# Performance work log

Hardware: AMD Instinct MI355X
Metric: run time of the kernel (lower is better)

Reference implementation:

```python
import jax, jax.numpy as jnp
import numpy as np

B, S = 64, 32
VF, IF = 512, 256
F = VF + IF        # fused feature dim == sensory dim
U = 768            # wiring units == rnn_hidden_dim (motor_size == units)
UNFOLDS = 6        # ncps LTC default ode_unfolds
EPS = 1e-8


def setup_inputs() -> dict:
    key = jax.random.key(0)
    ks = jax.random.split(key, 24)
    d = {}
    d['fv'] = jax.random.normal(ks[0], (B, S, VF), jnp.float32)
    d['fv_alter'] = jax.random.normal(ks[1], (B, S, VF), jnp.float32)
    d['fi'] = jax.random.normal(ks[2], (B, S, IF), jnp.float32)
    d['dec'] = jax.random.normal(ks[3], (B, S, 2), jnp.float32)
    # strictly increasing timestamps so relative timespans are positive
    d['ts'] = jnp.cumsum(jax.random.uniform(ks[4], (B, S + 1), jnp.float32, 0.01, 0.1), axis=1)
    # LTC cell parameters (ncps init ranges), FullyConnected wiring -> dense masks of ones
    d['input_w'] = jnp.ones((F,), jnp.float32)
    d['input_b'] = jnp.zeros((F,), jnp.float32)
    d['sensory_mu'] = jax.random.uniform(ks[5], (F, U), jnp.float32, 0.3, 0.8)
    d['sensory_sigma'] = jax.random.uniform(ks[6], (F, U), jnp.float32, 3.0, 8.0)
    d['sensory_w'] = jax.random.uniform(ks[7], (F, U), jnp.float32, 0.001, 1.0)
    d['sensory_erev'] = jnp.sign(jax.random.normal(ks[8], (F, U), jnp.float32))
    d['mu'] = jax.random.uniform(ks[9], (U, U), jnp.float32, 0.3, 0.8)
    d['sigma'] = jax.random.uniform(ks[10], (U, U), jnp.float32, 3.0, 8.0)
    d['w'] = jax.random.uniform(ks[11], (U, U), jnp.float32, 0.001, 1.0)
    d['erev'] = jnp.sign(jax.random.normal(ks[12], (U, U), jnp.float32))
    d['gleak'] = jax.random.uniform(ks[13], (U,), jnp.float32, 0.001, 1.0)
    d['vleak'] = jax.random.uniform(ks[14], (U,), jnp.float32, -0.2, 0.2)
    d['cm'] = jax.random.uniform(ks[15], (U,), jnp.float32, 0.4, 0.6)
    d['output_w'] = jnp.ones((U,), jnp.float32)
    d['output_b'] = jnp.zeros((U,), jnp.float32)
    d['W1'] = jax.random.normal(ks[16], (U, 128), jnp.float32) / np.sqrt(U)
    d['b1'] = jnp.zeros((128,), jnp.float32)
    d['W2'] = jax.random.normal(ks[17], (128, 6), jnp.float32) / np.sqrt(128.0)
    d['b2'] = jnp.zeros((6,), jnp.float32)
    return d


def _ltc(fused, rel_ts, input_w, input_b, sensory_mu, sensory_sigma, sensory_w,
         sensory_erev, mu, sigma, w, erev, gleak, vleak, cm, output_w, output_b):
    b = fused.shape[0]
    h0 = jnp.zeros((b, U), fused.dtype)

    def step(v, xs):
        inp, elapsed = xs  # (B,F), (B,)
        x = inp * input_w + input_b
        # sensory synapse activations: (B, F, U)
        s_act = sensory_w * jax.nn.sigmoid(sensory_sigma * (x[:, :, None] - sensory_mu))
        w_num_s = jnp.einsum('bfu,fu->bu', s_act, sensory_erev)
        w_den_s = jnp.sum(s_act, axis=1)
        cm_t = cm / (elapsed[:, None] / UNFOLDS)  # (B,U)

        def unfold(vv, _):
            act = w * jax.nn.sigmoid(sigma * (vv[:, :, None] - mu))  # (B,U,U)
            num = jnp.einsum('buv,uv->bv', act, erev) + w_num_s
            den = jnp.sum(act, axis=1) + w_den_s
            vv = (cm_t * vv + gleak * vleak + num) / (cm_t + gleak + den + EPS)
            return vv, None

        v, _ = jax.lax.scan(unfold, v, None, length=UNFOLDS)
        out = v * output_w + output_b  # motor_size == units
        return v, out

    _, outs = jax.lax.scan(step, h0, (jnp.swapaxes(fused, 0, 1), rel_ts.T))
    return jnp.swapaxes(outs, 0, 1), h0  # (B,S,U)


def reference(fv, fv_alter, fi, dec, ts, input_w, input_b, sensory_mu, sensory_sigma,
              sensory_w, sensory_erev, mu, sigma, w, erev, gleak, vleak, cm,
              output_w, output_b, W1, b1, W2, b2):
    fused = jnp.concatenate([fv, fi], axis=-1)  # FusionModule 'cat'
    rel_ts = ts[:, 1:] - ts[:, :-1]
    h_seq, h0 = _ltc(fused, rel_ts, input_w, input_b, sensory_mu, sensory_sigma,
                     sensory_w, sensory_erev, mu, sigma, w, erev, gleak, vleak, cm,
                     output_w, output_b)
    x = (h_seq - h0[:, None, :]) @ W1 + b1
    x = jnp.where(x > 0, x, 0.1 * x)  # LeakyReLU(0.1)
    pose = x @ W2 + b2
    return pose[:, None], h_seq  # (B,1,S,6), (B,S,U)
```

## Files before the change

### kernel.cpp

```cpp
#include <hip/hip_runtime.h>

#define Bq 64
#define Sq 32
#define VFq 512
#define IFq 256
#define Fq 768
#define Uq 768
#define UNFq 6
#define L2E 1.44269504088896340736f

template <int CTRL>
__device__ __forceinline__ float dpp_add(float x) {
  int t = __builtin_amdgcn_update_dpp(0, __builtin_bit_cast(int, x), CTRL, 0xF, 0xF, true);
  return x + __builtin_bit_cast(float, t);
}
__device__ __forceinline__ float swz_add4(float x) {
  int t = __builtin_amdgcn_ds_swizzle(__builtin_bit_cast(int, x), 0x101F);
  return x + __builtin_bit_cast(float, t);
}

__global__ __launch_bounds__(256) void k_prep(
    const float* __restrict__ smu, const float* __restrict__ ssig,
    const float* __restrict__ sw,  const float* __restrict__ ser,
    const float* __restrict__ rmu, const float* __restrict__ rsig,
    const float* __restrict__ rw,  const float* __restrict__ rer,
    const float* __restrict__ ts,
    float4* __restrict__ Ps, float4* __restrict__ Pr,
    float* __restrict__ iel, unsigned* __restrict__ flags)
{
  int bid = blockIdx.x, tid = threadIdx.x;
  if (bid < 1152) {
    int set = bid / 576, tile = bid % 576;
    int tv = tile / 24, tu = tile % 24;
    const float* Amu = set ? rmu : smu;
    const float* Asg = set ? rsig : ssig;
    const float* Aw  = set ? rw  : sw;
    const float* Aer = set ? rer : ser;
    float4* P = set ? Pr : Ps;
    __shared__ float4 tl[32][33];
    int cu = tid & 31, r0 = tid >> 5;
    for (int rr = 0; rr < 32; rr += 8) {
      int v = tv*32 + r0 + rr, u = tu*32 + cu;
      int idx = v*Uq + u;
      float sg = Asg[idx], m = Amu[idx], ww = Aw[idx], er = Aer[idx];
      tl[cu][r0+rr] = make_float4(-sg*L2E, sg*m*L2E, ww, ww*er);
    }
    __syncthreads();
    for (int rr = 0; rr < 32; rr += 8) {
      int u = tu*32 + r0 + rr, v = tv*32 + (tid & 31);
      P[u*Fq + v] = tl[r0+rr][tid & 31];
    }
  } else {
    for (int i = tid; i < Bq*Sq; i += 256) {
      int b = i / Sq, t = i % Sq;
      iel[i] = (float)UNFq / (ts[b*(Sq+1)+t+1] - ts[b*(Sq+1)+t]);
    }
    for (int i = tid; i < 512; i += 256) flags[i] = 0u;
  }
}

__global__ __launch_bounds__(768) void k_sensory(
    const float* __restrict__ fv, const float* __restrict__ fi,
    const float* __restrict__ iw, const float* __restrict__ ib,
    const float4* __restrict__ Ps,
    float* __restrict__ wns, float* __restrict__ wds)
{
  __shared__ float xs[16][Fq];
  __shared__ float scr[12][8][33];
  int tid = threadIdx.x;
  int bt_tile = blockIdx.x >> 6;
  int ut = blockIdx.x & 63;
  int u0 = ut * 12, bt0 = bt_tile * 16;
  {
    float wv = iw[tid], bv = ib[tid];
    for (int j = 0; j < 16; ++j) {
      int bt = bt0 + j, b = bt >> 5, t = bt & 31;
      float raw = (tid < VFq) ? fv[(b*Sq + t)*VFq + tid]
                              : fi[(b*Sq + t)*IFq + (tid - VFq)];
      xs[j][tid] = raw * wv + bv;
    }
  }
  __syncthreads();
  int w = tid >> 6, l = tid & 63;
  const float4* P = Ps + (u0 + w)*Fq;
  #pragma unroll
  for (int pass = 0; pass < 4; ++pass) {
    float num[4], den[4];
    #pragma unroll
    for (int q = 0; q < 4; ++q) { num[q] = 0.f; den[q] = 0.f; }
    for (int i = 0; i < 12; ++i) {
      int f = l + 64*i;
      float4 p = P[f];
      #pragma unroll
      for (int q = 0; q < 4; ++q) {
        float arg = fmaf(p.x, xs[4*pass + q][f], p.y);
        float e = __builtin_amdgcn_exp2f(arg);
        float r = __builtin_amdgcn_rcpf(1.0f + e);
        den[q] = fmaf(p.z, r, den[q]);
        num[q] = fmaf(p.w, r, num[q]);
      }
    }
    #pragma unroll
    for (int q = 0; q < 4; ++q) {
      num[q] = dpp_add<0xB1>(num[q]); den[q] = dpp_add<0xB1>(den[q]);
      num[q] = dpp_add<0x4E>(num[q]); den[q] = dpp_add<0x4E>(den[q]);
      num[q] = swz_add4(num[q]);      den[q] = swz_add4(den[q]);
    }
    if ((l & 7) == 0) {
      int rep = l >> 3;
      #pragma unroll
      for (int q = 0; q < 4; ++q) {
        scr[w][rep][4*pass + q] = num[q];
        scr[w][rep][16 + 4*pass + q] = den[q];
      }
    }
    __builtin_amdgcn_sched_barrier(0);
  }
  __syncthreads();
  if (tid < 192) {
    int u = tid >> 4, j = tid & 15;
    float nt = 0.f, dt = 0.f;
    #pragma unroll
    for (int rep = 0; rep < 8; ++rep) { nt += scr[u][rep][j]; dt += scr[u][rep][16+j]; }
    int bt = bt0 + j, b = bt >> 5, t = bt & 31;
    wns[(t*Bq + b)*Uq + (u0 + u)] = nt;
    wds[(t*Bq + b)*Uq + (u0 + u)] = dt;
  }
}

__global__ __launch_bounds__(768)
void k_recurrent(
    const float4* __restrict__ Pr,
    const float* __restrict__ wns, const float* __restrict__ wds,
    float* __restrict__ vg, const float* __restrict__ iel,
    unsigned* __restrict__ flags,
    const float* __restrict__ gleak, const float* __restrict__ vleak,
    const float* __restrict__ cm, const float* __restrict__ ow,
    const float* __restrict__ ob, float* __restrict__ hout)
{
  __shared__ float4 vvP[4][Uq];
  __shared__ float2 scr2[12][8][9];
  __shared__ float sinv[16][Sq];
  __shared__ float swn[2][96], swd[2][96];
  __shared__ float sgl[12], sglvl[12], scm[12], sow[12], sob[12];
  int tid = threadIdx.x;
  int g = blockIdx.x >> 6;
  int ut = blockIdx.x & 63;
  int u0 = ut*12, b0 = g*16;
  if (tid < 512) { int j = tid >> 5, t = tid & 31; sinv[j][t] = iel[(b0+j)*Sq + t]; }
  if (tid < 12) {
    float gl0 = gleak[u0+tid];
    sgl[tid] = gl0; sglvl[tid] = gl0 * vleak[u0+tid];
    scm[tid] = cm[u0+tid]; sow[tid] = ow[u0+tid]; sob[tid] = ob[u0+tid];
  }
  #pragma unroll
  for (int p = 0; p < 4; ++p) vvP[p][tid] = make_float4(0.f, 0.f, 0.f, 0.f);
  int w = tid >> 6, l = tid & 63;
  float4 Prg[12];
  #pragma unroll
  for (int i = 0; i < 12; ++i) Prg[i] = Pr[(u0 + w)*Uq + l + 64*i];
  __syncthreads();
  int uu = tid >> 3, jv = tid & 7;
  int p = 1;
  for (int t = 0; t < Sq; ++t) {
    if (tid < 96) {
      swn[0][tid] = wns[(t*Bq + b0 + jv)*Uq + u0 + uu];
      swd[0][tid] = wds[(t*Bq + b0 + jv)*Uq + u0 + uu];
      swn[1][tid] = wns[(t*Bq + b0 + 8 + jv)*Uq + u0 + uu];
      swd[1][tid] = wds[(t*Bq + b0 + 8 + jv)*Uq + u0 + uu];
    }
    for (int k = 0; k < UNFq; ++k, ++p) {
      int sp = p & 1, rp = sp ^ 1;
      #pragma unroll
      for (int h = 0; h < 2; ++h) {
        if (p > 1) {
          const unsigned* f = flags + (h*4 + g)*64 + l;
          unsigned tgt = (unsigned)(p - 1);
          while (true) {
            unsigned vf = __hip_atomic_load(f, __ATOMIC_RELAXED, __HIP_MEMORY_SCOPE_AGENT);
            if (__ballot(vf < tgt) == 0ull) break;
            __builtin_amdgcn_s_sleep(1);
          }
          const unsigned long long* src = (const unsigned long long*)
              (vg + (((rp*2 + h)*4 + g)*Uq + tid)*8);
          float2 tmp[4];
          #pragma unroll
          for (int q = 0; q < 4; ++q) {
            unsigned long long uq = __hip_atomic_load(src + q, __ATOMIC_RELAXED,
                                                      __HIP_MEMORY_SCOPE_AGENT);
            tmp[q] = __builtin_bit_cast(float2, uq);
          }
          vvP[2*h+0][tid] = make_float4(tmp[0].x, tmp[0].y, tmp[1].x, tmp[1].y);
          vvP[2*h+1][tid] = make_float4(tmp[2].x, tmp[2].y, tmp[3].x, tmp[3].y);
        }
        __syncthreads();
        #pragma unroll
        for (int pass = 0; pass < 2; ++pass) {
          int pn = 2*h + pass;
          float num[4], den[4];
          #pragma unroll
          for (int q = 0; q < 4; ++q) { num[q] = 0.f; den[q] = 0.f; }
          #pragma unroll
          for (int i = 0; i < 12; ++i) {
            int v = l + 64*i;
            float4 pp = Prg[i];
            float4 y = vvP[pn][v];
            float a0 = fmaf(pp.x, y.x, pp.y);
            float a1 = fmaf(pp.x, y.y, pp.y);
            float a2 = fmaf(pp.x, y.z, pp.y);
            float a3 = fmaf(pp.x, y.w, pp.y);
            float r0 = __builtin_amdgcn_rcpf(1.0f + __builtin_amdgcn_exp2f(a0));
            float r1 = __builtin_amdgcn_rcpf(1.0f + __builtin_amdgcn_exp2f(a1));
            float r2 = __builtin_amdgcn_rcpf(1.0f + __builtin_amdgcn_exp2f(a2));
            float r3 = __builtin_amdgcn_rcpf(1.0f + __builtin_amdgcn_exp2f(a3));
            den[0] = fmaf(pp.z, r0, den[0]);
            num[0] = fmaf(pp.w, r0, num[0]);
            den[1] = fmaf(pp.z, r1, den[1]);
            num[1] = fmaf(pp.w, r1, num[1]);
            den[2] = fmaf(pp.z, r2, den[2]);
            num[2] = fmaf(pp.w, r2, num[2]);
            den[3] = fmaf(pp.z, r3, den[3]);
            num[3] = fmaf(pp.w, r3, num[3]);
          }
          #pragma unroll
          for (int q = 0; q < 4; ++q) {
            num[q] = dpp_add<0xB1>(num[q]); den[q] = dpp_add<0xB1>(den[q]);
            num[q] = dpp_add<0x4E>(num[q]); den[q] = dpp_add<0x4E>(den[q]);
            num[q] = swz_add4(num[q]);      den[q] = swz_add4(den[q]);
          }
          if ((l & 7) == 0) {
            int r = l >> 3;
            #pragma unroll
            for (int q = 0; q < 4; ++q)
              scr2[w][r][4*pass + q] = make_float2(num[q], den[q]);
          }
          __builtin_amdgcn_sched_barrier(0);
        }
        __syncthreads();
        if (tid < 96) {
          float nt = swn[h][tid], dt = swd[h][tid];
          #pragma unroll
          for (int r = 0; r < 8; ++r) { float2 s = scr2[uu][r][jv]; nt += s.x; dt += s.y; }
          int jh = h*8 + jv;
          float cmt = scm[uu] * sinv[jh][t];
          const float* vrow = (const float*)&vvP[2*h + (jv >> 2)][u0 + uu];
          float vold = vrow[jv & 3];
          float vnew = (cmt*vold + sglvl[uu] + nt)
                     * __builtin_amdgcn_rcpf(cmt + sgl[uu] + dt + 1e-8f);
          __hip_atomic_store(&vg[(((sp*2 + h)*4 + g)*Uq + u0 + uu)*8 + jv], vnew,
                             __ATOMIC_RELAXED, __HIP_MEMORY_SCOPE_AGENT);
          if (k == UNFq-1)
            hout[((b0 + jh)*Sq + t)*Uq + u0 + uu] = fmaf(vnew, sow[uu], sob[uu]);
        }
        __builtin_amdgcn_s_waitcnt(0);
        __syncthreads();
        if (tid == 0)
          __hip_atomic_store(&flags[(h*4 + g)*64 + ut], (unsigned)p,
                             __ATOMIC_RELAXED, __HIP_MEMORY_SCOPE_AGENT);
      }
    }
  }
}

__global__ __launch_bounds__(128) void k_head(
    const float* __restrict__ hseq, const float* __restrict__ W1,
    const float* __restrict__ b1, const float* __restrict__ W2,
    const float* __restrict__ b2, float* __restrict__ pose)
{
  __shared__ float h[Uq];
  __shared__ float x1[128];
  int bt = blockIdx.x, tid = threadIdx.x;
  for (int j = 0; j < 6; ++j) h[tid + 128*j] = hseq[bt*Uq + tid + 128*j];
  __syncthreads();
  float acc = b1[tid];
  for (int f = 0; f < Uq; ++f) acc = fmaf(h[f], W1[f*128 + tid], acc);
  x1[tid] = acc > 0.f ? acc : 0.1f*acc;
  __syncthreads();
  if (tid < 6) {
    float a2 = b2[tid];
    #pragma unroll
    for (int c = 0; c < 128; ++c) a2 = fmaf(x1[c], W2[c*6 + tid], a2);
    pose[bt*6 + tid] = a2;
  }
}

extern "C" void kernel_launch(void* const* d_in, const int* in_sizes, int n_in,
                              void* d_out, int out_size, void* d_ws, size_t ws_size,
                              hipStream_t stream) {
  const float* fv   = (const float*)d_in[0];
  const float* fi   = (const float*)d_in[2];
  const float* ts   = (const float*)d_in[4];
  const float* iw   = (const float*)d_in[5];
  const float* ibb  = (const float*)d_in[6];
  const float* smu  = (const float*)d_in[7];
  const float* ssig = (const float*)d_in[8];
  const float* sw   = (const float*)d_in[9];
  const float* ser  = (const float*)d_in[10];
  const float* rmu  = (const float*)d_in[11];
  const float* rsig = (const float*)d_in[12];
  const float* rw   = (const float*)d_in[13];
  const float* rer  = (const float*)d_in[14];
  const float* gl   = (const float*)d_in[15];
  const float* vl   = (const float*)d_in[16];
  const float* cm   = (const float*)d_in[17];
  const float* ow   = (const float*)d_in[18];
  const float* ob   = (const float*)d_in[19];
  const float* W1   = (const float*)d_in[20];
  const float* b1   = (const float*)d_in[21];
  const float* W2   = (const float*)d_in[22];
  const float* b2   = (const float*)d_in[23];

  float* pose = (float*)d_out;
  float* hseq = (float*)d_out + Bq*Sq*6;

  float* ws = (float*)d_ws;
  float4* Ps = (float4*)ws;
  float4* Pr = (float4*)(ws + 2359296);
  float* wns = ws + 4718592;
  float* wds = ws + 6291456;
  float* vg  = ws + 7864320;
  float* iel = ws + 7962624;
  unsigned* flags = (unsigned*)(ws + 7964672);

  k_prep<<<1153, 256, 0, stream>>>(smu, ssig, sw, ser, rmu, rsig, rw, rer,
                                   ts, Ps, Pr, iel, flags);
  k_sensory<<<8192, 768, 0, stream>>>(fv, fi, iw, ibb, Ps, wns, wds);
  k_recurrent<<<256, 768, 0, stream>>>(Pr, wns, wds, vg, iel, flags,
                                       gl, vl, cm, ow, ob, hseq);
  k_head<<<2048, 128, 0, stream>>>(hseq, W1, b1, W2, b2, pose);
}
```

Baseline: 2.794 ms.

## Split recurrent kernel into more batch groups and share reciprocal across sigmoid pairs

The recurrent kernel now gives each block 8 batch rows instead of 16 and launches 512 blocks instead of 256. Each block does one pass per half instead of two, which shortens the serial per-unfold critical path, at the cost of more blocks polling flags and more grid-wide spin synchronisation. It also computes two sigmoids from a single reciprocal of the product (1+e0)(1+e1), trading one rcp for extra multiplies. The flag and state buffers are re-indexed to match the eight groups.

```diff
diff --git a/kernel.cpp b/kernel.cpp
--- a/kernel.cpp
+++ b/kernel.cpp
@@ -55,7 +55,7 @@
       int b = i / Sq, t = i % Sq;
       iel[i] = (float)UNFq / (ts[b*(Sq+1)+t+1] - ts[b*(Sq+1)+t]);
     }
-    for (int i = tid; i < 512; i += 256) flags[i] = 0u;
+    for (int i = tid; i < 1024; i += 256) flags[i] = 0u;
   }
 }
 
@@ -138,43 +138,43 @@
     const float* __restrict__ cm, const float* __restrict__ ow,
     const float* __restrict__ ob, float* __restrict__ hout)
 {
-  __shared__ float4 vvP[4][Uq];
-  __shared__ float2 scr2[12][8][9];
-  __shared__ float sinv[16][Sq];
-  __shared__ float swn[2][96], swd[2][96];
+  __shared__ float4 vvP[2][Uq];
+  __shared__ float2 scr2[12][8][5];
+  __shared__ float sinv[8][Sq];
+  __shared__ float swn[2][48], swd[2][48];
   __shared__ float sgl[12], sglvl[12], scm[12], sow[12], sob[12];
   int tid = threadIdx.x;
   int g = blockIdx.x >> 6;
   int ut = blockIdx.x & 63;
-  int u0 = ut*12, b0 = g*16;
-  if (tid < 512) { int j = tid >> 5, t = tid & 31; sinv[j][t] = iel[(b0+j)*Sq + t]; }
+  int u0 = ut*12, b0 = g*8;
+  if (tid < 256) { int j = tid >> 5, t = tid & 31; sinv[j][t] = iel[(b0+j)*Sq + t]; }
   if (tid < 12) {
     float gl0 = gleak[u0+tid];
     sgl[tid] = gl0; sglvl[tid] = gl0 * vleak[u0+tid];
     scm[tid] = cm[u0+tid]; sow[tid] = ow[u0+tid]; sob[tid] = ob[u0+tid];
   }
-  #pragma unroll
-  for (int p = 0; p < 4; ++p) vvP[p][tid] = make_float4(0.f, 0.f, 0.f, 0.f);
+  vvP[0][tid] = make_float4(0.f, 0.f, 0.f, 0.f);
+  vvP[1][tid] = make_float4(0.f, 0.f, 0.f, 0.f);
   int w = tid >> 6, l = tid & 63;
   float4 Prg[12];
   #pragma unroll
   for (int i = 0; i < 12; ++i) Prg[i] = Pr[(u0 + w)*Uq + l + 64*i];
   __syncthreads();
-  int uu = tid >> 3, jv = tid & 7;
+  int uu = tid >> 2, jv = tid & 3;
   int p = 1;
   for (int t = 0; t < Sq; ++t) {
-    if (tid < 96) {
+    if (tid < 48) {
       swn[0][tid] = wns[(t*Bq + b0 + jv)*Uq + u0 + uu];
       swd[0][tid] = wds[(t*Bq + b0 + jv)*Uq + u0 + uu];
-      swn[1][tid] = wns[(t*Bq + b0 + 8 + jv)*Uq + u0 + uu];
-      swd[1][tid] = wds[(t*Bq + b0 + 8 + jv)*Uq + u0 + uu];
+      swn[1][tid] = wns[(t*Bq + b0 + 4 + jv)*Uq + u0 + uu];
+      swd[1][tid] = wds[(t*Bq + b0 + 4 + jv)*Uq + u0 + uu];
     }
     for (int k = 0; k < UNFq; ++k, ++p) {
       int sp = p & 1, rp = sp ^ 1;
       #pragma unroll
       for (int h = 0; h < 2; ++h) {
         if (p > 1) {
-          const unsigned* f = flags + (h*4 + g)*64 + l;
+          const unsigned* f = flags + (h*8 + g)*64 + l;
           unsigned tgt = (unsigned)(p - 1);
           while (true) {
             unsigned vf = __hip_atomic_load(f, __ATOMIC_RELAXED, __HIP_MEMORY_SCOPE_AGENT);
@@ -182,21 +182,17 @@
             __builtin_amdgcn_s_sleep(1);
           }
           const unsigned long long* src = (const unsigned long long*)
-              (vg + (((rp*2 + h)*4 + g)*Uq + tid)*8);
-          float2 tmp[4];
-          #pragma unroll
-          for (int q = 0; q < 4; ++q) {
-            unsigned long long uq = __hip_atomic_load(src + q, __ATOMIC_RELAXED,
-                                                      __HIP_MEMORY_SCOPE_AGENT);
-            tmp[q] = __builtin_bit_cast(float2, uq);
-          }
-          vvP[2*h+0][tid] = make_float4(tmp[0].x, tmp[0].y, tmp[1].x, tmp[1].y);
-          vvP[2*h+1][tid] = make_float4(tmp[2].x, tmp[2].y, tmp[3].x, tmp[3].y);
+              (vg + (((rp*2 + h)*8 + g)*Uq + tid)*4);
+          unsigned long long q0 = __hip_atomic_load(src + 0, __ATOMIC_RELAXED,
+                                                    __HIP_MEMORY_SCOPE_AGENT);
+          unsigned long long q1 = __hip_atomic_load(src + 1, __ATOMIC_RELAXED,
+                                                    __HIP_MEMORY_SCOPE_AGENT);
+          float2 t0 = __builtin_bit_cast(float2, q0);
+          float2 t1 = __builtin_bit_cast(float2, q1);
+          vvP[h][tid] = make_float4(t0.x, t0.y, t1.x, t1.y);
         }
         __syncthreads();
-        #pragma unroll
-        for (int pass = 0; pass < 2; ++pass) {
-          int pn = 2*h + pass;
+        {
           float num[4], den[4];
           #pragma unroll
           for (int q = 0; q < 4; ++q) { num[q] = 0.f; den[q] = 0.f; }
@@ -204,23 +200,23 @@
           for (int i = 0; i < 12; ++i) {
             int v = l + 64*i;
             float4 pp = Prg[i];
-            float4 y = vvP[pn][v];
-            float a0 = fmaf(pp.x, y.x, pp.y);
-            float a1 = fmaf(pp.x, y.y, pp.y);
-            float a2 = fmaf(pp.x, y.z, pp.y);
-            float a3 = fmaf(pp.x, y.w, pp.y);
-            float r0 = __builtin_amdgcn_rcpf(1.0f + __builtin_amdgcn_exp2f(a0));
-            float r1 = __builtin_amdgcn_rcpf(1.0f + __builtin_amdgcn_exp2f(a1));
-            float r2 = __builtin_amdgcn_rcpf(1.0f + __builtin_amdgcn_exp2f(a2));
-            float r3 = __builtin_amdgcn_rcpf(1.0f + __builtin_amdgcn_exp2f(a3));
-            den[0] = fmaf(pp.z, r0, den[0]);
-            num[0] = fmaf(pp.w, r0, num[0]);
-            den[1] = fmaf(pp.z, r1, den[1]);
-            num[1] = fmaf(pp.w, r1, num[1]);
-            den[2] = fmaf(pp.z, r2, den[2]);
-            num[2] = fmaf(pp.w, r2, num[2]);
-            den[3] = fmaf(pp.z, r3, den[3]);
-            num[3] = fmaf(pp.w, r3, num[3]);
+            float4 y = vvP[h][v];
+            float e0 = 1.0f + __builtin_amdgcn_exp2f(fmaf(pp.x, y.x, pp.y));
+            float e1 = 1.0f + __builtin_amdgcn_exp2f(fmaf(pp.x, y.y, pp.y));
+            float e2 = 1.0f + __builtin_amdgcn_exp2f(fmaf(pp.x, y.z, pp.y));
+            float e3 = 1.0f + __builtin_amdgcn_exp2f(fmaf(pp.x, y.w, pp.y));
+            float r01 = __builtin_amdgcn_rcpf(e0 * e1);
+            float r23 = __builtin_amdgcn_rcpf(e2 * e3);
+            float s0 = r01 * e1, s1 = r01 * e0;
+            float s2 = r23 * e3, s3 = r23 * e2;
+            den[0] = fmaf(pp.z, s0, den[0]);
+            num[0] = fmaf(pp.w, s0, num[0]);
+            den[1] = fmaf(pp.z, s1, den[1]);
+            num[1] = fmaf(pp.w, s1, num[1]);
+            den[2] = fmaf(pp.z, s2, den[2]);
+            num[2] = fmaf(pp.w, s2, num[2]);
+            den[3] = fmaf(pp.z, s3, den[3]);
+            num[3] = fmaf(pp.w, s3, num[3]);
           }
           #pragma unroll
           for (int q = 0; q < 4; ++q) {
@@ -232,22 +228,22 @@
             int r = l >> 3;
             #pragma unroll
             for (int q = 0; q < 4; ++q)
-              scr2[w][r][4*pass + q] = make_float2(num[q], den[q]);
+              scr2[w][r][q] = make_float2(num[q], den[q]);
           }
           __builtin_amdgcn_sched_barrier(0);
         }
         __syncthreads();
-        if (tid < 96) {
+        if (tid < 48) {
           float nt = swn[h][tid], dt = swd[h][tid];
           #pragma unroll
           for (int r = 0; r < 8; ++r) { float2 s = scr2[uu][r][jv]; nt += s.x; dt += s.y; }
-          int jh = h*8 + jv;
+          int jh = h*4 + jv;
           float cmt = scm[uu] * sinv[jh][t];
-          const float* vrow = (const float*)&vvP[2*h + (jv >> 2)][u0 + uu];
-          float vold = vrow[jv & 3];
+          const float* vrow = (const float*)&vvP[h][u0 + uu];
+          float vold = vrow[jv];
           float vnew = (cmt*vold + sglvl[uu] + nt)
                      * __builtin_amdgcn_rcpf(cmt + sgl[uu] + dt + 1e-8f);
-          __hip_atomic_store(&vg[(((sp*2 + h)*4 + g)*Uq + u0 + uu)*8 + jv], vnew,
+          __hip_atomic_store(&vg[(((sp*2 + h)*8 + g)*Uq + u0 + uu)*4 + jv], vnew,
                              __ATOMIC_RELAXED, __HIP_MEMORY_SCOPE_AGENT);
           if (k == UNFq-1)
             hout[((b0 + jh)*Sq + t)*Uq + u0 + uu] = fmaf(vnew, sow[uu], sob[uu]);
@@ -255,7 +251,7 @@
         __builtin_amdgcn_s_waitcnt(0);
         __syncthreads();
         if (tid == 0)
-          __hip_atomic_store(&flags[(h*4 + g)*64 + ut], (unsigned)p,
+          __hip_atomic_store(&flags[(h*8 + g)*64 + ut], (unsigned)p,
                              __ATOMIC_RELAXED, __HIP_MEMORY_SCOPE_AGENT);
       }
     }
@@ -325,7 +321,7 @@
   k_prep<<<1153, 256, 0, stream>>>(smu, ssig, sw, ser, rmu, rsig, rw, rer,
                                    ts, Ps, Pr, iel, flags);
   k_sensory<<<8192, 768, 0, stream>>>(fv, fi, iw, ibb, Ps, wns, wds);
-  k_recurrent<<<256, 768, 0, stream>>>(Pr, wns, wds, vg, iel, flags,
+  k_recurrent<<<512, 768, 0, stream>>>(Pr, wns, wds, vg, iel, flags,
                                        gl, vl, cm, ow, ob, hseq);
   k_head<<<2048, 128, 0, stream>>>(hseq, W1, b1, W2, b2, pose);
 }
```

Measured after the change: 3.115 ms. +11.5%, slower.

## Overlap cross-block state fetch of next half with current half compute

Applied to the files above, without the earlier changes.

Restructures the recurrent unfold loop so that, while one half-batch's sigmoid reduction runs, the kernel waits on the other half's completion flags and issues its global state loads. The fetched values are written to shared memory only after the second pass, which hides the inter-block synchronization latency behind compute. The global state buffer changes from double buffering to one slot per half, and the flag layout and targets change to match. This adds more live registers and relies on a subtler ordering of flag checks to avoid reading stale or overwritten state.

```diff
diff --git a/kernel.cpp b/kernel.cpp
--- a/kernel.cpp
+++ b/kernel.cpp
@@ -8,6 +8,7 @@
 #define Uq 768
 #define UNFq 6
 #define L2E 1.44269504088896340736f
+typedef unsigned long long ull;
 
 template <int CTRL>
 __device__ __forceinline__ float dpp_add(float x) {
@@ -55,7 +56,7 @@
       int b = i / Sq, t = i % Sq;
       iel[i] = (float)UNFq / (ts[b*(Sq+1)+t+1] - ts[b*(Sq+1)+t]);
     }
-    for (int i = tid; i < 512; i += 256) flags[i] = 0u;
+    for (int i = tid; i < 1024; i += 256) flags[i] = 0u;
   }
 }
 
@@ -154,108 +155,126 @@
     scm[tid] = cm[u0+tid]; sow[tid] = ow[u0+tid]; sob[tid] = ob[u0+tid];
   }
   #pragma unroll
-  for (int p = 0; p < 4; ++p) vvP[p][tid] = make_float4(0.f, 0.f, 0.f, 0.f);
+  for (int q = 0; q < 4; ++q) vvP[q][tid] = make_float4(0.f, 0.f, 0.f, 0.f);
   int w = tid >> 6, l = tid & 63;
   float4 Prg[12];
   #pragma unroll
   for (int i = 0; i < 12; ++i) Prg[i] = Pr[(u0 + w)*Uq + l + 64*i];
   __syncthreads();
-  int uu = tid >> 3, jv = tid & 7;
-  int p = 1;
+  int uu8 = tid >> 3, jv = tid & 7;
   for (int t = 0; t < Sq; ++t) {
     if (tid < 96) {
-      swn[0][tid] = wns[(t*Bq + b0 + jv)*Uq + u0 + uu];
-      swd[0][tid] = wds[(t*Bq + b0 + jv)*Uq + u0 + uu];
-      swn[1][tid] = wns[(t*Bq + b0 + 8 + jv)*Uq + u0 + uu];
-      swd[1][tid] = wds[(t*Bq + b0 + 8 + jv)*Uq + u0 + uu];
-    }
-    for (int k = 0; k < UNFq; ++k, ++p) {
-      int sp = p & 1, rp = sp ^ 1;
+      swn[0][tid] = wns[(t*Bq + b0 + jv)*Uq + u0 + uu8];
+      swd[0][tid] = wds[(t*Bq + b0 + jv)*Uq + u0 + uu8];
+      swn[1][tid] = wns[(t*Bq + b0 + 8 + jv)*Uq + u0 + uu8];
+      swd[1][tid] = wds[(t*Bq + b0 + 8 + jv)*Uq + u0 + uu8];
+    }
+    for (int k = 0; k < UNFq; ++k) {
+      int p = t*UNFq + k;
       #pragma unroll
       for (int h = 0; h < 2; ++h) {
-        if (p > 1) {
-          const unsigned* f = flags + (h*4 + g)*64 + l;
-          unsigned tgt = (unsigned)(p - 1);
+        int hp = 1 - h;
+        float num0[4], den0[4], num1[4], den1[4];
+        #pragma unroll
+        for (int q = 0; q < 4; ++q) { num0[q] = 0.f; den0[q] = 0.f; }
+        #pragma unroll
+        for (int i = 0; i < 12; ++i) {
+          int v = l + 64*i;
+          float4 pp = Prg[i];
+          float4 y = vvP[2*h][v];
+          float r0 = __builtin_amdgcn_rcpf(1.0f + __builtin_amdgcn_exp2f(fmaf(pp.x, y.x, pp.y)));
+          float r1 = __builtin_amdgcn_rcpf(1.0f + __builtin_amdgcn_exp2f(fmaf(pp.x, y.y, pp.y)));
+          float r2 = __builtin_amdgcn_rcpf(1.0f + __builtin_amdgcn_exp2f(fmaf(pp.x, y.z, pp.y)));
+          float r3 = __builtin_amdgcn_rcpf(1.0f + __builtin_amdgcn_exp2f(fmaf(pp.x, y.w, pp.y)));
+          den0[0] = fmaf(pp.z, r0, den0[0]); num0[0] = fmaf(pp.w, r0, num0[0]);
+          den0[1] = fmaf(pp.z, r1, den0[1]); num0[1] = fmaf(pp.w, r1, num0[1]);
+          den0[2] = fmaf(pp.z, r2, den0[2]); num0[2] = fmaf(pp.w, r2, num0[2]);
+          den0[3] = fmaf(pp.z, r3, den0[3]); num0[3] = fmaf(pp.w, r3, num0[3]);
+        }
+        #pragma unroll
+        for (int q = 0; q < 4; ++q) {
+          num0[q] = dpp_add<0xB1>(num0[q]); den0[q] = dpp_add<0xB1>(den0[q]);
+          num0[q] = dpp_add<0x4E>(num0[q]); den0[q] = dpp_add<0x4E>(den0[q]);
+          num0[q] = swz_add4(num0[q]);      den0[q] = swz_add4(den0[q]);
+        }
+        if ((l & 7) == 0) {
+          int r = l >> 3;
+          #pragma unroll
+          for (int q = 0; q < 4; ++q) scr2[w][r][q] = make_float2(num0[q], den0[q]);
+        }
+        __builtin_amdgcn_sched_barrier(0);
+        ull ga0 = 0, ga1 = 0, ga2 = 0, ga3 = 0;
+        bool do_g = !(p == 0 && h == 0);
+        if (do_g) {
+          const unsigned* f = flags + hp*256 + g*64 + l;
+          unsigned tgt = (unsigned)(p + h);
           while (true) {
             unsigned vf = __hip_atomic_load(f, __ATOMIC_RELAXED, __HIP_MEMORY_SCOPE_AGENT);
             if (__ballot(vf < tgt) == 0ull) break;
             __builtin_amdgcn_s_sleep(1);
           }
-          const unsigned long long* src = (const unsigned long long*)
-              (vg + (((rp*2 + h)*4 + g)*Uq + tid)*8);
-          float2 tmp[4];
+          const ull* src = (const ull*)(vg + (hp*4 + g)*Uq*8) + tid*4;
+          ga0 = __hip_atomic_load(src + 0, __ATOMIC_RELAXED, __HIP_MEMORY_SCOPE_AGENT);
+          ga1 = __hip_atomic_load(src + 1, __ATOMIC_RELAXED, __HIP_MEMORY_SCOPE_AGENT);
+          ga2 = __hip_atomic_load(src + 2, __ATOMIC_RELAXED, __HIP_MEMORY_SCOPE_AGENT);
+          ga3 = __hip_atomic_load(src + 3, __ATOMIC_RELAXED, __HIP_MEMORY_SCOPE_AGENT);
+        }
+        __builtin_amdgcn_sched_barrier(0);
+        #pragma unroll
+        for (int q = 0; q < 4; ++q) { num1[q] = 0.f; den1[q] = 0.f; }
+        #pragma unroll
+        for (int i = 0; i < 12; ++i) {
+          int v = l + 64*i;
+          float4 pp = Prg[i];
+          float4 y = vvP[2*h+1][v];
+          float r0 = __builtin_amdgcn_rcpf(1.0f + __builtin_amdgcn_exp2f(fmaf(pp.x, y.x, pp.y)));
+          float r1 = __builtin_amdgcn_rcpf(1.0f + __builtin_amdgcn_exp2f(fmaf(pp.x, y.y, pp.y)));
+          float r2 = __builtin_amdgcn_rcpf(1.0f + __builtin_amdgcn_exp2f(fmaf(pp.x, y.z, pp.y)));
+          float r3 = __builtin_amdgcn_rcpf(1.0f + __builtin_amdgcn_exp2f(fmaf(pp.x, y.w, pp.y)));
+          den1[0] = fmaf(pp.z, r0, den1[0]); num1[0] = fmaf(pp.w, r0, num1[0]);
+          den1[1] = fmaf(pp.z, r1, den1[1]); num1[1] = fmaf(pp.w, r1, num1[1]);
+          den1[2] = fmaf(pp.z, r2, den1[2]); num1[2] = fmaf(pp.w, r2, num1[2]);
+          den1[3] = fmaf(pp.z, r3, den1[3]); num1[3] = fmaf(pp.w, r3, num1[3]);
+        }
+        #pragma unroll
+        for (int q = 0; q < 4; ++q) {
+          num1[q] = dpp_add<0xB1>(num1[q]); den1[q] = dpp_add<0xB1>(den1[q]);
+          num1[q] = dpp_add<0x4E>(num1[q]); den1[q] = dpp_add<0x4E>(den1[q]);
+          num1[q] = swz_add4(num1[q]);      den1[q] = swz_add4(den1[q]);
+        }
+        if ((l & 7) == 0) {
+          int r = l >> 3;
           #pragma unroll
-          for (int q = 0; q < 4; ++q) {
-            unsigned long long uq = __hip_atomic_load(src + q, __ATOMIC_RELAXED,
-                                                      __HIP_MEMORY_SCOPE_AGENT);
-            tmp[q] = __builtin_bit_cast(float2, uq);
-          }
-          vvP[2*h+0][tid] = make_float4(tmp[0].x, tmp[0].y, tmp[1].x, tmp[1].y);
-          vvP[2*h+1][tid] = make_float4(tmp[2].x, tmp[2].y, tmp[3].x, tmp[3].y);
-        }
-        __syncthreads();
-        #pragma unroll
-        for (int pass = 0; pass < 2; ++pass) {
-          int pn = 2*h + pass;
-          float num[4], den[4];
-          #pragma unroll
-          for (int q = 0; q < 4; ++q) { num[q] = 0.f; den[q] = 0.f; }
-          #pragma unroll
-          for (int i = 0; i < 12; ++i) {
-            int v = l + 64*i;
-            float4 pp = Prg[i];
-            float4 y = vvP[pn][v];
-            float a0 = fmaf(pp.x, y.x, pp.y);
-            float a1 = fmaf(pp.x, y.y, pp.y);
-            float a2 = fmaf(pp.x, y.z, pp.y);
-            float a3 = fmaf(pp.x, y.w, pp.y);
-            float r0 = __builtin_amdgcn_rcpf(1.0f + __builtin_amdgcn_exp2f(a0));
-            float r1 = __builtin_amdgcn_rcpf(1.0f + __builtin_amdgcn_exp2f(a1));
-            float r2 = __builtin_amdgcn_rcpf(1.0f + __builtin_amdgcn_exp2f(a2));
-            float r3 = __builtin_amdgcn_rcpf(1.0f + __builtin_amdgcn_exp2f(a3));
-            den[0] = fmaf(pp.z, r0, den[0]);
-            num[0] = fmaf(pp.w, r0, num[0]);
-            den[1] = fmaf(pp.z, r1, den[1]);
-            num[1] = fmaf(pp.w, r1, num[1]);
-            den[2] = fmaf(pp.z, r2, den[2]);
-            num[2] = fmaf(pp.w, r2, num[2]);
-            den[3] = fmaf(pp.z, r3, den[3]);
-            num[3] = fmaf(pp.w, r3, num[3]);
-          }
-          #pragma unroll
-          for (int q = 0; q < 4; ++q) {
-            num[q] = dpp_add<0xB1>(num[q]); den[q] = dpp_add<0xB1>(den[q]);
-            num[q] = dpp_add<0x4E>(num[q]); den[q] = dpp_add<0x4E>(den[q]);
-            num[q] = swz_add4(num[q]);      den[q] = swz_add4(den[q]);
-          }
-          if ((l & 7) == 0) {
-            int r = l >> 3;
-            #pragma unroll
-            for (int q = 0; q < 4; ++q)
-              scr2[w][r][4*pass + q] = make_float2(num[q], den[q]);
-          }
-          __builtin_amdgcn_sched_barrier(0);
+          for (int q = 0; q < 4; ++q) scr2[w][r][4+q] = make_float2(num1[q], den1[q]);
+        }
+        if (do_g) {
+          float2 t0 = __builtin_bit_cast(float2, ga0);
+          float2 t1 = __builtin_bit_cast(float2, ga1);
+          float2 t2 = __builtin_bit_cast(float2, ga2);
+          float2 t3 = __builtin_bit_cast(float2, ga3);
+          vvP[2*hp+0][tid] = make_float4(t0.x, t0.y, t1.x, t1.y);
+          vvP[2*hp+1][tid] = make_float4(t2.x, t2.y, t3.x, t3.y);
         }
         __syncthreads();
         if (tid < 96) {
           float nt = swn[h][tid], dt = swd[h][tid];
           #pragma unroll
-          for (int r = 0; r < 8; ++r) { float2 s = scr2[uu][r][jv]; nt += s.x; dt += s.y; }
+          for (int r = 0; r < 8; ++r) { float2 s = scr2[uu8][r][jv]; nt += s.x; dt += s.y; }
           int jh = h*8 + jv;
-          float cmt = scm[uu] * sinv[jh][t];
-          const float* vrow = (const float*)&vvP[2*h + (jv >> 2)][u0 + uu];
+          float cmt = scm[uu8] * sinv[jh][t];
+          const float* vrow = (const float*)&vvP[2*h + (jv >> 2)][u0 + uu8];
           float vold = vrow[jv & 3];
-          float vnew = (cmt*vold + sglvl[uu] + nt)
-                     * __builtin_amdgcn_rcpf(cmt + sgl[uu] + dt + 1e-8f);
-          __hip_atomic_store(&vg[(((sp*2 + h)*4 + g)*Uq + u0 + uu)*8 + jv], vnew,
+          float vnew = (cmt*vold + sglvl[uu8] + nt)
+                     * __builtin_amdgcn_rcpf(cmt + sgl[uu8] + dt + 1e-8f);
+          __hip_atomic_store(&vg[(h*4 + g)*Uq*8 + (u0 + uu8)*8 + jv], vnew,
                              __ATOMIC_RELAXED, __HIP_MEMORY_SCOPE_AGENT);
           if (k == UNFq-1)
-            hout[((b0 + jh)*Sq + t)*Uq + u0 + uu] = fmaf(vnew, sow[uu], sob[uu]);
+            hout[((b0 + jh)*Sq + t)*Uq + u0 + uu8] = fmaf(vnew, sow[uu8], sob[uu8]);
         }
         __builtin_amdgcn_s_waitcnt(0);
         __syncthreads();
         if (tid == 0)
-          __hip_atomic_store(&flags[(h*4 + g)*64 + ut], (unsigned)p,
+          __hip_atomic_store(&flags[h*256 + g*64 + ut], (unsigned)(p + 1),
                              __ATOMIC_RELAXED, __HIP_MEMORY_SCOPE_AGENT);
       }
     }
```

Result: faster. 2.425 ms (-13.2%).
